# Kernel optimization log

Hardware: AMD Instinct MI355X
Metric: run time of the kernel (lower is better)

## Reference

```python
import jax, jax.numpy as jnp
import numpy as np

B, H, W, DIM, HEADS, WS, SHIFT = 16, 64, 64, 512, 16, 8, 4
HEAD_DIM = DIM // HEADS
MLP_HID = 4 * DIM
N_WIN = (H // WS) * (W // WS)
NW = WS * WS  # tokens per window
SCALE = HEAD_DIM ** -0.5
LN_EPS = 1e-5


def _np_win_partition(x, ws):
    # replicates rearrange 'b (s1 h2) (s2 w2) c -> (b h2 w2) (s1 s2) c' (interleaved partition)
    b, h, w, c = x.shape
    h2, w2 = h // ws, w // ws
    x = x.reshape(b, ws, h2, ws, w2, c).transpose(0, 2, 4, 1, 3, 5)
    return x.reshape(b * h2 * w2, ws * ws, c)


def _build_mask():
    img = np.zeros((1, H, W, 1), np.float32)
    sl = [slice(0, -WS), slice(-WS, -SHIFT), slice(-SHIFT, None)]
    cnt = 0
    for hs in sl:
        for ws_ in sl:
            img[:, hs, ws_, :] = cnt
            cnt += 1
    wm = _np_win_partition(img, WS).reshape(-1, NW)  # (N_WIN, NW)
    diff = wm[:, None, :] - wm[:, :, None]
    mask = np.where(diff == 0, 1.0, 0.0).astype(np.float32)
    return (1.0 - mask) * -1e10  # (N_WIN, NW, NW) additive mask


def _rel_index():
    ch = np.arange(WS)
    coords = np.stack(np.meshgrid(ch, ch, indexing='ij')).reshape(2, -1)  # (2, NW)
    rel = (coords[:, :, None] - coords[:, None, :]).transpose(1, 2, 0)  # (NW, NW, 2)
    rel[..., 0] += WS - 1
    rel[..., 1] += WS - 1
    rel[..., 0] *= 2 * WS - 1
    return rel.sum(-1)  # (NW, NW) int


MASK = jnp.asarray(_build_mask())
REL_IDX = jnp.asarray(_rel_index().reshape(-1))


def _win_partition(x):  # (B, H, W, C) -> (B*N_WIN, NW, C)
    h2, w2 = H // WS, W // WS
    x = x.reshape(B, WS, h2, WS, w2, DIM).transpose(0, 2, 4, 1, 3, 5)
    return x.reshape(B * h2 * w2, WS * WS, DIM)


def _win_reverse(w):  # (B*N_WIN, NW, C) -> (B, H*W, C), inverse of the interleaved partition
    h2, w2 = H // WS, W // WS
    x = w.reshape(B, h2, w2, WS, WS, DIM).transpose(0, 3, 1, 4, 2, 5)
    return x.reshape(B, H * W, DIM)


def _ln(x, w, b):
    m = x.mean(-1, keepdims=True)
    v = jnp.mean((x - m) ** 2, axis=-1, keepdims=True)
    return (x - m) / jnp.sqrt(v + LN_EPS) * w + b


def setup_inputs() -> dict:
    key = jax.random.key(0)
    ks = jax.random.split(key, 6)
    std = 0.02
    return {
        'x': jax.random.normal(ks[0], (B, H * W, DIM), jnp.float32),
        'ln1_w': jnp.ones((DIM,), jnp.float32),
        'ln1_b': jnp.zeros((DIM,), jnp.float32),
        'qkv_w': jax.random.normal(ks[1], (3 * DIM, DIM), jnp.float32) * std,
        'qkv_b': jnp.zeros((3 * DIM,), jnp.float32),
        'rpb_table': jax.random.normal(ks[2], ((2 * WS - 1) ** 2, HEADS), jnp.float32) * std,
        'proj_w': jax.random.normal(ks[3], (DIM, DIM), jnp.float32) * std,
        'proj_b': jnp.zeros((DIM,), jnp.float32),
        'ln2_w': jnp.ones((DIM,), jnp.float32),
        'ln2_b': jnp.zeros((DIM,), jnp.float32),
        'fc1_w': jax.random.normal(ks[4], (MLP_HID, DIM), jnp.float32) * std,
        'fc1_b': jnp.zeros((MLP_HID,), jnp.float32),
        'fc2_w': jax.random.normal(ks[5], (DIM, MLP_HID), jnp.float32) * std,
        'fc2_b': jnp.zeros((DIM,), jnp.float32),
    }


def reference(x, ln1_w, ln1_b, qkv_w, qkv_b, rpb_table, proj_w, proj_b,
              ln2_w, ln2_b, fc1_w, fc1_b, fc2_w, fc2_b):
    h = x
    y = _ln(x, ln1_w, ln1_b).reshape(B, H, W, DIM)
    y = jnp.roll(y, (-SHIFT, -SHIFT), axis=(1, 2))  # cyclic shift
    xw = _win_partition(y)  # (B*N_WIN, NW, DIM)

    qkv = xw @ qkv_w.T + qkv_b  # (B*N_WIN, NW, 3*DIM)
    # original splits channel as (heads, head_dim, qkv) with qkv innermost
    qkv = qkv.reshape(B * N_WIN, NW, HEADS, HEAD_DIM, 3)
    q = qkv[..., 0].transpose(0, 2, 1, 3) * SCALE  # (Bw, H, NW, d)
    k = qkv[..., 1].transpose(0, 2, 1, 3)
    v = qkv[..., 2].transpose(0, 2, 1, 3)

    attn = jnp.einsum('bhqd,bhkd->bhqk', q, k)
    bias = rpb_table[REL_IDX].reshape(NW, NW, HEADS).transpose(2, 0, 1)  # (H, NW, NW)
    attn = attn + bias[None]
    # shift mask: per-window additive mask broadcast over batch and heads
    attn = attn.reshape(B, N_WIN, HEADS, NW, NW) + MASK[None, :, None]
    attn = jax.nn.softmax(attn, axis=-1).reshape(B * N_WIN, HEADS, NW, NW)

    out = jnp.einsum('bhqk,bhkd->bhqd', attn, v)
    out = out.transpose(0, 2, 1, 3).reshape(B * N_WIN, NW, DIM)
    out = out @ proj_w.T + proj_b

    attn_out = _win_reverse(out)  # (B, H*W, DIM)
    # NOTE: faithful to original - attention output is NOT rolled back before residual
    x2 = h + attn_out

    z = _ln(x2, ln2_w, ln2_b)
    z = jax.nn.gelu(z @ fc1_w.T + fc1_b, approximate=False)
    z = z @ fc2_w.T + fc2_b
    return x2 + z
```

## Files before the change

kernel.cpp:

```cpp
#include <hip/hip_runtime.h>
#include <math.h>

typedef short short8 __attribute__((ext_vector_type(8)));
typedef float f32x4 __attribute__((ext_vector_type(4)));
typedef unsigned short u16;
typedef u16 us4 __attribute__((ext_vector_type(4)));

#define DEVI static __device__ __forceinline__

constexpr float SCALE_Q = 0.17677669529663687f;

DEVI u16 f2bf(float f) {
  unsigned u = __builtin_bit_cast(unsigned, f);
  u += 0x7FFFu + ((u >> 16) & 1u);
  return (u16)(u >> 16);
}

DEVI void gload16(const u16* g, u16* l) {
  __builtin_amdgcn_global_load_lds((const __attribute__((address_space(1))) void*)g,
                                   (__attribute__((address_space(3))) void*)l,
                                   16, 0, 0);
}

DEVI short8 ldsw(const u16* base, int r, int g) {
  return *(const short8*)(base + r * 32 + (((g + (r >> 1)) & 3) << 3));
}

__global__ void cvt_bf16(const float4* __restrict__ src, us4* __restrict__ dst, int n4) {
  int i = blockIdx.x * 256 + threadIdx.x;
  if (i < n4) {
    float4 v = src[i];
    us4 o = { f2bf(v.x), f2bf(v.y), f2bf(v.z), f2bf(v.w) };
    dst[i] = o;
  }
}

__global__ void cvt_qkvw(const float4* __restrict__ src, us4* __restrict__ dst) {
  int i = blockIdx.x * 256 + threadIdx.x;
  int row = i >> 7, c4 = i & 127;
  int which = row >> 9, head = (row >> 5) & 15, d = row & 31;
  int srow = head * 96 + d * 3 + which;
  float4 v = src[srow * 128 + c4];
  us4 o = { f2bf(v.x), f2bf(v.y), f2bf(v.z), f2bf(v.w) };
  dst[i] = o;
}

__global__ void perm_qkvb(const float* __restrict__ src, float* __restrict__ dst) {
  int i = blockIdx.x * 256 + threadIdx.x;
  int which = i >> 9, head = (i >> 5) & 15, d = i & 31;
  dst[i] = src[head * 96 + d * 3 + which];
}

template<bool PERM>
__global__ __launch_bounds__(256) void ln_kernel(const float* __restrict__ src,
                                                 const float* __restrict__ gw,
                                                 const float* __restrict__ gb,
                                                 u16* __restrict__ dst) {
  int wid = threadIdx.x >> 6, lane = threadIdx.x & 63;
  int m = blockIdx.x * 4 + wid;
  int srow;
  if (PERM) {
    int b = m >> 12;
    int win = (m >> 6) & 63, t = m & 63;
    int i2 = win >> 3, j2 = win & 7, s1 = t >> 3, s2 = t & 7;
    int h = (s1 * 8 + i2 + 4) & 63, w = (s2 * 8 + j2 + 4) & 63;
    srow = (b << 12) + h * 64 + w;
  } else {
    srow = m;
  }
  const float4* r4 = (const float4*)(src + (size_t)srow * 512);
  float4 v0 = r4[lane], v1 = r4[lane + 64];
  float s  = v0.x + v0.y + v0.z + v0.w + v1.x + v1.y + v1.z + v1.w;
  float ss = v0.x*v0.x + v0.y*v0.y + v0.z*v0.z + v0.w*v0.w
           + v1.x*v1.x + v1.y*v1.y + v1.z*v1.z + v1.w*v1.w;
  #pragma unroll
  for (int off = 1; off < 64; off <<= 1) {
    s  += __shfl_xor(s, off);
    ss += __shfl_xor(ss, off);
  }
  float mean = s * (1.f/512.f);
  float var  = ss * (1.f/512.f) - mean*mean;
  float rstd = rsqrtf(var + 1e-5f);
  const float4* w4 = (const float4*)gw;
  const float4* b4 = (const float4*)gb;
  float4 wa = w4[lane], ba = b4[lane], wb = w4[lane+64], bb = b4[lane+64];
  us4 o0 = { f2bf((v0.x-mean)*rstd*wa.x + ba.x),
             f2bf((v0.y-mean)*rstd*wa.y + ba.y),
             f2bf((v0.z-mean)*rstd*wa.z + ba.z),
             f2bf((v0.w-mean)*rstd*wa.w + ba.w) };
  us4 o1 = { f2bf((v1.x-mean)*rstd*wb.x + bb.x),
             f2bf((v1.y-mean)*rstd*wb.y + bb.y),
             f2bf((v1.z-mean)*rstd*wb.z + bb.z),
             f2bf((v1.w-mean)*rstd*wb.w + bb.w) };
  us4* d4 = (us4*)(dst + (size_t)m * 512);
  d4[lane] = o0; d4[lane + 64] = o1;
}

template<int MODE, int NT>
__global__ __launch_bounds__(256, 4) void gemm_k(const u16* __restrict__ A,
                                                 const u16* __restrict__ Bw,
                                                 const float* __restrict__ bias,
                                                 u16* __restrict__ o0, u16* __restrict__ o1,
                                                 u16* __restrict__ o2,
                                                 float* __restrict__ fo,
                                                 const float* __restrict__ resid,
                                                 int M, int N) {
  const int K = NT * 32;
  __shared__ u16 LDS[3][2][4096];
  int nt = N >> 7;
  int nwg = gridDim.x, cpx = nwg >> 3, bid = blockIdx.x;
  int swz = (bid & 7) * cpx + (bid >> 3);
  int tm = swz / nt, tn = swz % nt;
  int tid = threadIdx.x, lane = tid & 63, wv = tid >> 6;
  int wm = wv >> 1, wn = wv & 1;
  int rr = lane & 15, g = lane >> 4;

  int srow = tid >> 2;
  int sch = (((tid & 3) - (srow >> 1)) & 3) << 3;
  const u16* a0 = A  + (size_t)(tm * 128 + srow) * K + sch;
  const u16* b0 = Bw + (size_t)(tn * 128 + srow) * K + sch;
  size_t k64 = (size_t)64 * K;

#define STG(buf, kt) { \
    u16* dA = &LDS[buf][0][0] + (wv << 9); u16* dB = &LDS[buf][1][0] + (wv << 9); \
    gload16(a0 + (kt) * 32, dA); gload16(a0 + k64 + (kt) * 32, dA + 2048); \
    gload16(b0 + (kt) * 32, dB); gload16(b0 + k64 + (kt) * 32, dB + 2048); }

  f32x4 acc[4][4] = {};

  STG(0, 0); STG(1, 1);
  asm volatile("s_waitcnt vmcnt(4)" ::: "memory");
  __builtin_amdgcn_s_barrier();

  #pragma unroll
  for (int kt = 0; kt < NT; ++kt) {
    const int cur = kt % 3;
    const int nb = (kt + 2) % 3;
    if (kt + 2 < NT) STG(nb, kt + 2);
    const u16* AT = &LDS[cur][0][0];
    const u16* BT = &LDS[cur][1][0];
    short8 af[4], bf[4];
    #pragma unroll
    for (int mi = 0; mi < 4; mi++) af[mi] = ldsw(AT, wm*64 + mi*16 + rr, g);
    #pragma unroll
    for (int ni = 0; ni < 4; ni++) bf[ni] = ldsw(BT, wn*64 + ni*16 + rr, g);
    __builtin_amdgcn_s_setprio(1);
    #pragma unroll
    for (int mi = 0; mi < 4; mi++)
      #pragma unroll
      for (int ni = 0; ni < 4; ni++)
        acc[mi][ni] = __builtin_amdgcn_mfma_f32_16x16x32_bf16(af[mi], bf[ni], acc[mi][ni], 0, 0, 0);
    __builtin_amdgcn_s_setprio(0);
    if (kt + 2 < NT) { asm volatile("s_waitcnt vmcnt(4)" ::: "memory"); }
    else             { asm volatile("s_waitcnt vmcnt(0)" ::: "memory"); }
    __builtin_amdgcn_s_barrier();
  }
#undef STG

  __syncthreads();
  u16* wreg = &LDS[0][0][0] + wv * 4096;
  int rb0 = tm * 128 + wm * 64;
  int cb0 = tn * 128 + wn * 64;

  if (MODE == 0 || MODE == 2) {
    bool isV = (MODE == 0) && (tn >= 8);
    if (!isV) {
      #pragma unroll
      for (int mi = 0; mi < 4; mi++)
        #pragma unroll
        for (int ni = 0; ni < 4; ni++) {
          float bv = bias[cb0 + ni * 16 + rr];
          #pragma unroll
          for (int r = 0; r < 4; r++) {
            float val = acc[mi][ni][r] + bv;
            if (MODE == 2) {
              float u = val * (0.79788456f + 0.03567740814f * val * val);
              float e = __expf(2.f * u);
              val = val * (1.f - __builtin_amdgcn_rcpf(e + 1.f));
            }
            if (MODE == 0 && tn < 4) val *= SCALE_Q;
            int row = mi * 16 + g * 4 + r;
            int col = ni * 16 + rr;
            wreg[row * 64 + (((col >> 3) ^ (row & 7)) << 3) + (col & 7)] = f2bf(val);
          }
        }
      int row = lane;
      #pragma unroll
      for (int chk = 0; chk < 8; chk++) {
        short8 vd = *(const short8*)&wreg[row * 64 + ((chk ^ (row & 7)) << 3)];
        if (MODE == 2) {
          size_t grow = (size_t)rb0 + row;
          *(short8*)(o0 + grow * N + cb0 + chk * 8) = vd;
        } else {
          int grow = rb0 + row;
          int w = grow >> 6, tt = grow & 63;
          int colp = (tn & 3) * 128 + wn * 64 + chk * 8;
          int head = colp >> 5;
          u16* dst = (tn < 4) ? o0 : o1;
          *(short8*)(dst + ((size_t)(w * 16 + head) * 64 + tt) * 32 + (colp & 31)) = vd;
        }
      }
    } else {
      #pragma unroll
      for (int mi = 0; mi < 4; mi++)
        #pragma unroll
        for (int ni = 0; ni < 4; ni++) {
          float bv = bias[cb0 + ni * 16 + rr];
          #pragma unroll
          for (int r = 0; r < 4; r++) {
            float val = acc[mi][ni][r] + bv;
            int row = mi * 16 + g * 4 + r;
            int col = ni * 16 + rr;
            wreg[col * 64 + (((row >> 3) ^ (col & 7)) << 3) + (row & 7)] = f2bf(val);
          }
        }
      int cb0v = cb0 - 1024;
      int col = lane;
      int head = (cb0v + col) >> 5, d = (cb0v + col) & 31;
      int w = rb0 >> 6;
      #pragma unroll
      for (int chk = 0; chk < 8; chk++) {
        short8 vd = *(const short8*)&wreg[col * 64 + ((chk ^ (col & 7)) << 3)];
        *(short8*)(o2 + ((size_t)(w * 16 + head) * 32 + d) * 64 + chk * 8) = vd;
      }
    }
  } else {
    #pragma unroll
    for (int ni = 0; ni < 4; ni++) {
      int col = cb0 + ni * 16 + rr;
      float bv = bias[col];
      #pragma unroll
      for (int mi = 0; mi < 4; mi++) {
        #pragma unroll
        for (int r = 0; r < 4; r++) {
          int row = rb0 + mi * 16 + g * 4 + r;
          float val = acc[mi][ni][r] + bv;
          if (MODE == 1) {
            int w = row >> 6, t = row & 63;
            int b = w >> 6, win = w & 63;
            int i2 = win >> 3, j2 = win & 7, s1 = t >> 3, s2 = t & 7;
            int pos = (b << 12) + (s1 * 8 + i2) * 64 + (s2 * 8 + j2);
            size_t idx = (size_t)pos * 512 + col;
            fo[idx] = resid[idx] + val;
          } else {
            size_t idx = (size_t)row * 512 + col;
            fo[idx] += val;
          }
        }
      }
    }
  }
}

DEVI int zone1(int x) { return x < 56 ? 0 : (x < 60 ? 1 : 2); }

__global__ __launch_bounds__(256) void attn_k(const u16* __restrict__ qb,
                                              const u16* __restrict__ kb,
                                              const u16* __restrict__ vtb,
                                              const float* __restrict__ rpb,
                                              u16* __restrict__ outb) {
  __shared__ u16 P[4][64][72];
  int wid = threadIdx.x >> 6, lane = threadIdx.x & 63;
  int p = blockIdx.x * 4 + wid;
  int w = p >> 4, head = p & 15;
  const u16* qq = qb  + (size_t)p * 2048;
  const u16* kk = kb  + (size_t)p * 2048;
  const u16* vv = vtb + (size_t)p * 2048;
  int rr = lane & 15, g = lane >> 4;

  short8 qf[4], kf[4];
  #pragma unroll
  for (int i = 0; i < 4; i++) qf[i] = *(const short8*)(qq + (i*16 + rr)*32 + g*8);
  #pragma unroll
  for (int i = 0; i < 4; i++) kf[i] = *(const short8*)(kk + (i*16 + rr)*32 + g*8);

  f32x4 zero = {0.f, 0.f, 0.f, 0.f};
  f32x4 s[4][4];
  #pragma unroll
  for (int qi = 0; qi < 4; qi++)
    #pragma unroll
    for (int kj = 0; kj < 4; kj++)
      s[qi][kj] = __builtin_amdgcn_mfma_f32_16x16x32_bf16(qf[qi], kf[kj], zero, 0, 0, 0);

  int win = w & 63, i2 = win >> 3, j2 = win & 7;
  #pragma unroll
  for (int qi = 0; qi < 4; qi++) {
    #pragma unroll
    for (int r = 0; r < 4; r++) {
      int i = qi*16 + g*4 + r;
      int s1i = i >> 3, s2i = i & 7;
      int zi = zone1(s1i*8 + i2)*3 + zone1(s2i*8 + j2);
      #pragma unroll
      for (int kj = 0; kj < 4; kj++) {
        int j = kj*16 + rr;
        int s1j = j >> 3, s2j = j & 7;
        float bv = rpb[((s1i - s1j + 7)*15 + (s2i - s2j + 7))*16 + head];
        int zj = zone1(s1j*8 + i2)*3 + zone1(s2j*8 + j2);
        s[qi][kj][r] += bv + (zi != zj ? -1e10f : 0.f);
      }
    }
  }

  float inv[4][4];
  #pragma unroll
  for (int qi = 0; qi < 4; qi++) {
    #pragma unroll
    for (int r = 0; r < 4; r++) {
      float mx = fmaxf(fmaxf(s[qi][0][r], s[qi][1][r]), fmaxf(s[qi][2][r], s[qi][3][r]));
      mx = fmaxf(mx, __shfl_xor(mx, 1));
      mx = fmaxf(mx, __shfl_xor(mx, 2));
      mx = fmaxf(mx, __shfl_xor(mx, 4));
      mx = fmaxf(mx, __shfl_xor(mx, 8));
      float sum = 0.f;
      #pragma unroll
      for (int kj = 0; kj < 4; kj++) {
        float e = __expf(s[qi][kj][r] - mx);
        s[qi][kj][r] = e;
        sum += e;
      }
      sum += __shfl_xor(sum, 1);
      sum += __shfl_xor(sum, 2);
      sum += __shfl_xor(sum, 4);
      sum += __shfl_xor(sum, 8);
      inv[qi][r] = 1.f / sum;
    }
  }

  #pragma unroll
  for (int qi = 0; qi < 4; qi++)
    #pragma unroll
    for (int kj = 0; kj < 4; kj++)
      #pragma unroll
      for (int r = 0; r < 4; r++)
        P[wid][qi*16 + g*4 + r][kj*16 + rr] = f2bf(s[qi][kj][r]);

  f32x4 o[4][2] = {};
  #pragma unroll
  for (int jh = 0; jh < 2; jh++) {
    short8 vf[2];
    #pragma unroll
    for (int df = 0; df < 2; df++)
      vf[df] = *(const short8*)(vv + (size_t)(df*16 + rr)*64 + jh*32 + g*8);
    #pragma unroll
    for (int qi = 0; qi < 4; qi++) {
      short8 pf = *(const short8*)(&P[wid][qi*16 + rr][jh*32 + g*8]);
      #pragma unroll
      for (int df = 0; df < 2; df++)
        o[qi][df] = __builtin_amdgcn_mfma_f32_16x16x32_bf16(pf, vf[df], o[qi][df], 0, 0, 0);
    }
  }

  #pragma unroll
  for (int qi = 0; qi < 4; qi++)
    #pragma unroll
    for (int df = 0; df < 2; df++)
      #pragma unroll
      for (int r = 0; r < 4; r++) {
        int t = qi*16 + g*4 + r;
        int d = df*16 + rr;
        outb[(size_t)(w*64 + t)*512 + head*32 + d] = f2bf(o[qi][df][r] * inv[qi][r]);
      }
}

extern "C" void kernel_launch(void* const* d_in, const int* in_sizes, int n_in,
                              void* d_out, int out_size, void* d_ws, size_t ws_size,
                              hipStream_t stream) {
  const float* x     = (const float*)d_in[0];
  const float* ln1w  = (const float*)d_in[1];
  const float* ln1b  = (const float*)d_in[2];
  const float* qkvw  = (const float*)d_in[3];
  const float* qkvb  = (const float*)d_in[4];
  const float* rpb   = (const float*)d_in[5];
  const float* projw = (const float*)d_in[6];
  const float* projb = (const float*)d_in[7];
  const float* ln2w  = (const float*)d_in[8];
  const float* ln2b  = (const float*)d_in[9];
  const float* fc1w  = (const float*)d_in[10];
  const float* fc1b  = (const float*)d_in[11];
  const float* fc2w  = (const float*)d_in[12];
  const float* fc2b  = (const float*)d_in[13];
  float* out = (float*)d_out;

  char* ws = (char*)d_ws;
  u16* wqkv  = (u16*)(ws + 0);
  u16* wproj = (u16*)(ws + 1572864);
  u16* wfc1  = (u16*)(ws + 2097152);
  u16* wfc2  = (u16*)(ws + 4194304);
  float* pb  = (float*)(ws + 6291456);
  size_t base = 8ull << 20;
  u16* xw = (u16*)(ws + base);
  u16* qb = (u16*)(ws + base + (64ull  << 20));
  u16* kb = (u16*)(ws + base + (128ull << 20));
  u16* vb = (u16*)(ws + base + (192ull << 20));
  u16* attnb = xw;
  u16* zb    = xw;
  u16* hb    = qb;

  cvt_qkvw<<<768, 256, 0, stream>>>((const float4*)qkvw, (us4*)wqkv);
  perm_qkvb<<<6, 256, 0, stream>>>(qkvb, pb);
  cvt_bf16<<<256,  256, 0, stream>>>((const float4*)projw, (us4*)wproj, 65536);
  cvt_bf16<<<1024, 256, 0, stream>>>((const float4*)fc1w,  (us4*)wfc1,  262144);
  cvt_bf16<<<1024, 256, 0, stream>>>((const float4*)fc2w,  (us4*)wfc2,  262144);

  ln_kernel<true><<<16384, 256, 0, stream>>>(x, ln1w, ln1b, xw);
  gemm_k<0, 16><<<6144, 256, 0, stream>>>(xw, wqkv, pb, qb, kb, vb, nullptr, nullptr,
                                          65536, 1536);
  attn_k<<<4096, 256, 0, stream>>>(qb, kb, vb, rpb, attnb);
  gemm_k<1, 16><<<2048, 256, 0, stream>>>(attnb, wproj, projb, nullptr, nullptr, nullptr,
                                          out, x, 65536, 512);
  ln_kernel<false><<<16384, 256, 0, stream>>>(out, ln2w, ln2b, zb);
  gemm_k<2, 16><<<8192, 256, 0, stream>>>(zb, wfc1, fc1b, hb, nullptr, nullptr, nullptr, nullptr,
                                          65536, 2048);
  gemm_k<3, 64><<<2048, 256, 0, stream>>>(hb, wfc2, fc2b, nullptr, nullptr, nullptr, out, nullptr,
                                          65536, 512);
}
```

Before: 894.6 us.

## Fuse fc1, GELU and fc2 into one MLP kernel keeping hidden in LDS

Replaces the separate fc1 (with GELU epilogue) and fc2 GEMM launches with a single fused_mlp kernel. Each 512-thread block loads a 64-row tile of the normalized input into LDS, computes the 2048-wide hidden activation in 256-column chunks, applies GELU and writes bf16 into a double-buffered LDS tile, then accumulates the fc2 product in registers before adding to the output. This removes the write and re-read of the large hidden activation through global memory. In exchange, every block streams the full fc1 and fc2 weights straight from global/L2 without LDS staging or prefetch, so weight traffic rises sharply. The large LDS footprint also limits occupancy.

```diff
diff --git a/kernel.cpp b/kernel.cpp
--- a/kernel.cpp
+++ b/kernel.cpp
@@ -14,6 +14,12 @@
   unsigned u = __builtin_bit_cast(unsigned, f);
   u += 0x7FFFu + ((u >> 16) & 1u);
   return (u16)(u >> 16);
+}
+
+DEVI float gelu_t(float val) {
+  float u = val * (0.79788456f + 0.03567740814f * val * val);
+  float e = __expf(2.f * u);
+  return val * (1.f - __builtin_amdgcn_rcpf(e + 1.f));
 }
 
 DEVI void gload16(const u16* g, u16* l) {
@@ -162,8 +168,8 @@
   int rb0 = tm * 128 + wm * 64;
   int cb0 = tn * 128 + wn * 64;
 
-  if (MODE == 0 || MODE == 2) {
-    bool isV = (MODE == 0) && (tn >= 8);
+  if (MODE == 0) {
+    bool isV = (tn >= 8);
     if (!isV) {
       #pragma unroll
       for (int mi = 0; mi < 4; mi++)
@@ -173,12 +179,7 @@
           #pragma unroll
           for (int r = 0; r < 4; r++) {
             float val = acc[mi][ni][r] + bv;
-            if (MODE == 2) {
-              float u = val * (0.79788456f + 0.03567740814f * val * val);
-              float e = __expf(2.f * u);
-              val = val * (1.f - __builtin_amdgcn_rcpf(e + 1.f));
-            }
-            if (MODE == 0 && tn < 4) val *= SCALE_Q;
+            if (tn < 4) val *= SCALE_Q;
             int row = mi * 16 + g * 4 + r;
             int col = ni * 16 + rr;
             wreg[row * 64 + (((col >> 3) ^ (row & 7)) << 3) + (col & 7)] = f2bf(val);
@@ -188,17 +189,12 @@
       #pragma unroll
       for (int chk = 0; chk < 8; chk++) {
         short8 vd = *(const short8*)&wreg[row * 64 + ((chk ^ (row & 7)) << 3)];
-        if (MODE == 2) {
-          size_t grow = (size_t)rb0 + row;
-          *(short8*)(o0 + grow * N + cb0 + chk * 8) = vd;
-        } else {
-          int grow = rb0 + row;
-          int w = grow >> 6, tt = grow & 63;
-          int colp = (tn & 3) * 128 + wn * 64 + chk * 8;
-          int head = colp >> 5;
-          u16* dst = (tn < 4) ? o0 : o1;
-          *(short8*)(dst + ((size_t)(w * 16 + head) * 64 + tt) * 32 + (colp & 31)) = vd;
-        }
+        int grow = rb0 + row;
+        int w = grow >> 6, tt = grow & 63;
+        int colp = (tn & 3) * 128 + wn * 64 + chk * 8;
+        int head = colp >> 5;
+        u16* dst = (tn < 4) ? o0 : o1;
+        *(short8*)(dst + ((size_t)(w * 16 + head) * 64 + tt) * 32 + (colp & 31)) = vd;
       }
     } else {
       #pragma unroll
@@ -235,20 +231,109 @@
         for (int r = 0; r < 4; r++) {
           int row = rb0 + mi * 16 + g * 4 + r;
           float val = acc[mi][ni][r] + bv;
-          if (MODE == 1) {
-            int w = row >> 6, t = row & 63;
-            int b = w >> 6, win = w & 63;
-            int i2 = win >> 3, j2 = win & 7, s1 = t >> 3, s2 = t & 7;
-            int pos = (b << 12) + (s1 * 8 + i2) * 64 + (s2 * 8 + j2);
-            size_t idx = (size_t)pos * 512 + col;
-            fo[idx] = resid[idx] + val;
-          } else {
-            size_t idx = (size_t)row * 512 + col;
-            fo[idx] += val;
-          }
+          int w = row >> 6, t = row & 63;
+          int b = w >> 6, win = w & 63;
+          int i2 = win >> 3, j2 = win & 7, s1 = t >> 3, s2 = t & 7;
+          int pos = (b << 12) + (s1 * 8 + i2) * 64 + (s2 * 8 + j2);
+          size_t idx = (size_t)pos * 512 + col;
+          fo[idx] = resid[idx] + val;
         }
       }
     }
+  }
+}
+
+__global__ __launch_bounds__(512, 2) void fused_mlp(const u16* __restrict__ z,
+                                                    const u16* __restrict__ W1,
+                                                    const u16* __restrict__ W2,
+                                                    const float* __restrict__ b1,
+                                                    const float* __restrict__ b2,
+                                                    float* __restrict__ out) {
+  __shared__ u16 As[32768];
+  __shared__ u16 Hb[2][16384];
+  int tid = threadIdx.x, lane = tid & 63, wv = tid >> 6;
+  int rr = lane & 15, g = lane >> 4;
+  int m0 = blockIdx.x * 64;
+
+  #pragma unroll
+  for (int l = 0; l < 8; l++) {
+    int L = l * 512 + tid;
+    int r = L >> 6, sck = L & 63;
+    gload16(z + (size_t)(m0 + r) * 512 + ((sck ^ (r & 7)) << 3), &As[L * 8]);
+  }
+  asm volatile("s_waitcnt vmcnt(0)" ::: "memory");
+  __builtin_amdgcn_s_barrier();
+
+  f32x4 acc2[4][4] = {};
+
+  #pragma unroll 2
+  for (int c = 0; c < 8; ++c) {
+    u16* H = &Hb[c & 1][0];
+    f32x4 acc1[4][2] = {};
+    int cb1 = c * 256 + wv * 32;
+    #pragma unroll
+    for (int st = 0; st < 16; ++st) {
+      short8 bf1[2], af1[4];
+      #pragma unroll
+      for (int ni = 0; ni < 2; ni++)
+        bf1[ni] = *(const short8*)(W1 + (size_t)(cb1 + ni * 16 + rr) * 512 + st * 32 + g * 8);
+      #pragma unroll
+      for (int mi = 0; mi < 4; mi++) {
+        int row = mi * 16 + rr;
+        af1[mi] = *(const short8*)(&As[row * 512 + (((st * 4 + g) ^ (row & 7)) << 3)]);
+      }
+      #pragma unroll
+      for (int mi = 0; mi < 4; mi++)
+        #pragma unroll
+        for (int ni = 0; ni < 2; ni++)
+          acc1[mi][ni] = __builtin_amdgcn_mfma_f32_16x16x32_bf16(af1[mi], bf1[ni], acc1[mi][ni], 0, 0, 0);
+    }
+    #pragma unroll
+    for (int ni = 0; ni < 2; ni++) {
+      int colg = wv * 32 + ni * 16 + rr;
+      float bv = b1[c * 256 + colg];
+      #pragma unroll
+      for (int mi = 0; mi < 4; mi++)
+        #pragma unroll
+        for (int q = 0; q < 4; q++) {
+          int row = mi * 16 + g * 4 + q;
+          float val = gelu_t(acc1[mi][ni][q] + bv);
+          H[row * 256 + (((colg >> 3) ^ (row & 7)) << 3) + (colg & 7)] = f2bf(val);
+        }
+    }
+    __syncthreads();
+    #pragma unroll
+    for (int st = 0; st < 8; ++st) {
+      short8 wb[4], ha[4];
+      #pragma unroll
+      for (int ni = 0; ni < 4; ni++)
+        wb[ni] = *(const short8*)(W2 + (size_t)(wv * 64 + ni * 16 + rr) * 2048 + c * 256 + st * 32 + g * 8);
+      #pragma unroll
+      for (int mi = 0; mi < 4; mi++) {
+        int row = mi * 16 + rr;
+        ha[mi] = *(const short8*)(&H[row * 256 + (((st * 4 + g) ^ (row & 7)) << 3)]);
+      }
+      __builtin_amdgcn_s_setprio(1);
+      #pragma unroll
+      for (int mi = 0; mi < 4; mi++)
+        #pragma unroll
+        for (int ni = 0; ni < 4; ni++)
+          acc2[mi][ni] = __builtin_amdgcn_mfma_f32_16x16x32_bf16(ha[mi], wb[ni], acc2[mi][ni], 0, 0, 0);
+      __builtin_amdgcn_s_setprio(0);
+    }
+  }
+
+  #pragma unroll
+  for (int ni = 0; ni < 4; ni++) {
+    int col = wv * 64 + ni * 16 + rr;
+    float bv = b2[col];
+    #pragma unroll
+    for (int mi = 0; mi < 4; mi++)
+      #pragma unroll
+      for (int q = 0; q < 4; q++) {
+        size_t idx = (size_t)(m0 + mi * 16 + g * 4 + q) * 512 + col;
+        out[idx] += acc2[mi][ni][q] + bv;
+      }
   }
 }
 
@@ -394,7 +479,6 @@
   u16* vb = (u16*)(ws + base + (192ull << 20));
   u16* attnb = xw;
   u16* zb    = xw;
-  u16* hb    = qb;
 
   cvt_qkvw<<<768, 256, 0, stream>>>((const float4*)qkvw, (us4*)wqkv);
   perm_qkvb<<<6, 256, 0, stream>>>(qkvb, pb);
@@ -409,8 +493,5 @@
   gemm_k<1, 16><<<2048, 256, 0, stream>>>(attnb, wproj, projb, nullptr, nullptr, nullptr,
                                           out, x, 65536, 512);
   ln_kernel<false><<<16384, 256, 0, stream>>>(out, ln2w, ln2b, zb);
-  gemm_k<2, 16><<<8192, 256, 0, stream>>>(zb, wfc1, fc1b, hb, nullptr, nullptr, nullptr, nullptr,
-                                          65536, 2048);
-  gemm_k<3, 64><<<2048, 256, 0, stream>>>(hb, wfc2, fc2b, nullptr, nullptr, nullptr, out, nullptr,
-                                          65536, 512);
-}
+  fused_mlp<<<1024, 512, 0, stream>>>(zb, wfc1, wfc2, fc1b, fc2b, out);
+}
```

Measured after the change: 984.7 us. 10.1% more time.
